# Kernel tuning notes

Hardware: AMD Instinct MI355X
Metric: run time of the kernel (lower is better)

The kernel has to match this reference:

```python
import jax, jax.numpy as jnp
import numpy as np

D_MODEL = 1024
NHEAD = 16
D_FF = 4096
LN_EPS = 1e-5


def _layer_norm(x, g, b):
    mu = jnp.mean(x, axis=-1, keepdims=True)
    var = jnp.mean(jnp.square(x - mu), axis=-1, keepdims=True)
    return (x - mu) * jax.lax.rsqrt(var + LN_EPS) * g + b


def setup_inputs() -> dict:
    key = jax.random.key(0)
    ks = jax.random.split(key, 12)
    d, f = D_MODEL, D_FF
    s = 1.0 / np.sqrt(d)
    inp = {
        "src": jax.random.normal(ks[0], (2, 2048, d), dtype=jnp.float32),
        "Wq": jax.random.uniform(ks[1], (d, d), jnp.float32, -s, s),
        "bq": jnp.zeros((d,), jnp.float32),
        "Wk": jax.random.uniform(ks[2], (d, d), jnp.float32, -s, s),
        "bk": jnp.zeros((d,), jnp.float32),
        "Wv": jax.random.uniform(ks[3], (d, d), jnp.float32, -s, s),
        "bv": jnp.zeros((d,), jnp.float32),
        "Wo": jax.random.uniform(ks[4], (d, d), jnp.float32, -s, s),
        "bo": jnp.zeros((d,), jnp.float32),
        "W1": jax.random.uniform(ks[5], (d, f), jnp.float32, -s, s),
        "b1": jnp.zeros((f,), jnp.float32),
        "W2": jax.random.uniform(ks[6], (f, d), jnp.float32, -1.0 / np.sqrt(f), 1.0 / np.sqrt(f)),
        "b2": jnp.zeros((d,), jnp.float32),
        "ln1_g": jnp.ones((d,), jnp.float32),
        "ln1_b": jnp.zeros((d,), jnp.float32),
        "ln2_g": jnp.ones((d,), jnp.float32),
        "ln2_b": jnp.zeros((d,), jnp.float32),
    }
    return inp


def reference(src, Wq, bq, Wk, bk, Wv, bv, Wo, bo, W1, b1, W2, b2,
              ln1_g, ln1_b, ln2_g, ln2_b):
    B, S, D = src.shape
    H = NHEAD
    hd = D // H
    # QKV projections, split into heads: [B, H, S, hd]
    q = (src @ Wq + bq).reshape(B, S, H, hd).transpose(0, 2, 1, 3)
    k = (src @ Wk + bk).reshape(B, S, H, hd).transpose(0, 2, 1, 3)
    v = (src @ Wv + bv).reshape(B, S, H, hd).transpose(0, 2, 1, 3)
    # Explicit full-score attention (no mask branch), as in source.
    scores = jnp.einsum("bhqd,bhkd->bhqk", q, k) / jnp.sqrt(jnp.asarray(hd, src.dtype))
    attn = jax.nn.softmax(scores, axis=-1)
    ctx = jnp.einsum("bhqk,bhkd->bhqd", attn, v)
    ctx = ctx.transpose(0, 2, 1, 3).reshape(B, S, D)
    src2 = ctx @ Wo + bo
    x = _layer_norm(src + src2, ln1_g, ln1_b)
    ff = jax.nn.relu(x @ W1 + b1) @ W2 + b2
    out = _layer_norm(x + ff, ln2_g, ln2_b)
    return out
```

## Files before the change

### kernel.cpp

```cpp
#include <hip/hip_runtime.h>
#include <cstdint>
#include <cstddef>

#define SEQ 2048
#define BATCH 2
#define ROWS (BATCH * SEQ)

typedef __attribute__((ext_vector_type(8))) short short8;
typedef __attribute__((ext_vector_type(4))) float f32x4;
typedef __attribute__((ext_vector_type(8))) _Float16 half8;
typedef __attribute__((ext_vector_type(2))) __fp16 fp16x2;

__device__ __forceinline__ unsigned short f2bf(float f) {
  union { float f; uint32_t u; } v; v.f = f;
  uint32_t r = v.u + 0x7fffu + ((v.u >> 16) & 1u);
  return (unsigned short)(r >> 16);
}

__device__ __forceinline__ unsigned short bf2h(unsigned short b) {
  union { uint32_t u; float f; } v; v.u = ((uint32_t)b) << 16;
  union { _Float16 h; unsigned short u; } o; o.h = (_Float16)v.f;
  return o.u;
}

__device__ __forceinline__ void async16(const void* g, void* l) {
  __builtin_amdgcn_global_load_lds((const __attribute__((address_space(1))) void*)g,
                                   (__attribute__((address_space(3))) void*)l, 16, 0, 0);
}

__global__ __launch_bounds__(256) void f2bf_kernel(const float* __restrict__ in,
                                                   unsigned short* __restrict__ out) {
  size_t i = ((size_t)blockIdx.x * 256 + threadIdx.x) * 4;
  float4 vv = *(const float4*)(in + i);
  ushort4 o;
  o.x = f2bf(vv.x); o.y = f2bf(vv.y); o.z = f2bf(vv.z); o.w = f2bf(vv.w);
  *(ushort4*)(out + i) = o;
}

__global__ __launch_bounds__(256) void wtrans(const float* __restrict__ W,
                                              unsigned short* __restrict__ WT,
                                              int K, int N, float scale) {
  __shared__ float t[32][33];
  int n0 = blockIdx.x * 32, k0 = blockIdx.y * 32;
  for (int i = threadIdx.y; i < 32; i += 8)
    t[i][threadIdx.x] = W[(size_t)(k0 + i) * N + n0 + threadIdx.x];
  __syncthreads();
  for (int i = threadIdx.y; i < 32; i += 8)
    WT[(size_t)(n0 + i) * K + k0 + threadIdx.x] = f2bf(t[threadIdx.x][i] * scale);
}

__global__ __launch_bounds__(256) void bias_concat(const float* __restrict__ bq,
                                                   const float* __restrict__ bk,
                                                   const float* __restrict__ bv,
                                                   float* __restrict__ o) {
  int i = blockIdx.x * 256 + threadIdx.x;
  float v = (i < 1024) ? bq[i] * 0.18033688f : (i < 2048 ? bk[i - 1024] : bv[i - 2048]);
  o[i] = v;
}

__global__ __launch_bounds__(256) void vtrans(const unsigned short* __restrict__ qkv,
                                              unsigned short* __restrict__ VT) {
  const int st = blockIdx.x, bh = blockIdx.y, b = bh >> 4, h = bh & 15;
  __shared__ unsigned short t[64][72];
  const int tid = threadIdx.x;
#pragma unroll
  for (int it = 0; it < 2; ++it) {
    int i = it * 256 + tid;
    int s = i >> 3, c = (i & 7) * 8;
    short8 v = *(const short8*)(qkv + ((size_t)b * SEQ + st * 64 + s) * 3072 + 2048 + h * 64 + c);
#pragma unroll
    for (int j = 0; j < 8; ++j) t[c + j][s] = bf2h((unsigned short)v[j]);
  }
  __syncthreads();
#pragma unroll
  for (int it = 0; it < 2; ++it) {
    int i = it * 256 + tid;
    int d = i >> 3, sc = (i & 7) * 8;
    short8 o;
#pragma unroll
    for (int j = 0; j < 8; ++j) o[j] = (short)t[d][sc + j];
    *(short8*)(VT + ((size_t)bh * 64 + d) * 2048 + st * 64 + sc) = o;
  }
}

template <bool RELU, bool OUTBF, bool HASRES>
__global__ __launch_bounds__(256) void gemm_bt(
    const unsigned short* __restrict__ A, const unsigned short* __restrict__ BT,
    const float* __restrict__ bias, const float* __restrict__ Rres,
    float* __restrict__ outF, unsigned short* __restrict__ outB,
    int M, int N, int K) {
  __shared__ unsigned short As[2][128 * 32];
  __shared__ unsigned short Bs[2][128 * 32];
  const int tid = threadIdx.x;
  const int lane = tid & 63, ln = lane & 15, quad = lane >> 4;
  const int w = tid >> 6;
  const int m0 = blockIdx.y * 128, n0 = blockIdx.x * 128;
  const int mw = (w >> 1) * 64, nw = (w & 1) * 64;
  f32x4 acc[4][4] = {};
  const int i0 = tid, i1 = tid + 256;
  const int r0 = i0 >> 2, kc0 = (i0 & 3) * 8;
  const int r1 = i1 >> 2, kc1 = (i1 & 3) * 8;
  for (int k0 = 0; k0 < K; k0 += 64) {
    __syncthreads();
#pragma unroll
    for (int p = 0; p < 2; ++p) {
      const int kp = k0 + p * 32;
      async16(A + (size_t)(m0 + r0) * K + kp + kc0, &As[p][i0 * 8]);
      async16(A + (size_t)(m0 + r1) * K + kp + kc1, &As[p][i1 * 8]);
      async16(BT + (size_t)(n0 + r0) * K + kp + kc0, &Bs[p][i0 * 8]);
      async16(BT + (size_t)(n0 + r1) * K + kp + kc1, &Bs[p][i1 * 8]);
    }
    __syncthreads();
#pragma unroll
    for (int p = 0; p < 2; ++p) {
      short8 a[4], b[4];
#pragma unroll
      for (int mi = 0; mi < 4; ++mi)
        a[mi] = *(const short8*)&As[p][(mw + mi * 16 + ln) * 32 + quad * 8];
#pragma unroll
      for (int ni = 0; ni < 4; ++ni)
        b[ni] = *(const short8*)&Bs[p][(nw + ni * 16 + ln) * 32 + quad * 8];
#pragma unroll
      for (int mi = 0; mi < 4; ++mi)
#pragma unroll
        for (int ni = 0; ni < 4; ++ni)
          acc[mi][ni] = __builtin_amdgcn_mfma_f32_16x16x32_bf16(a[mi], b[ni], acc[mi][ni], 0, 0, 0);
    }
  }
#pragma unroll
  for (int mi = 0; mi < 4; ++mi) {
#pragma unroll
    for (int ni = 0; ni < 4; ++ni) {
#pragma unroll
      for (int reg = 0; reg < 4; ++reg) {
        int row = m0 + mw + mi * 16 + quad * 4 + reg;
        int col = n0 + nw + ni * 16 + ln;
        float v = acc[mi][ni][reg] + bias[col];
        if (HASRES) v += Rres[(size_t)row * N + col];
        if (RELU) v = fmaxf(v, 0.f);
        if (OUTBF) outB[(size_t)row * N + col] = f2bf(v);
        else outF[(size_t)row * N + col] = v;
      }
    }
  }
}

template <bool RELU, bool OUTBF, bool HASRES>
__global__ __launch_bounds__(256) void gemm_bt64(
    const unsigned short* __restrict__ A, const unsigned short* __restrict__ BT,
    const float* __restrict__ bias, const float* __restrict__ Rres,
    float* __restrict__ outF, unsigned short* __restrict__ outB,
    int M, int N, int K) {
  __shared__ unsigned short As[4][128 * 32];
  __shared__ unsigned short Bs[4][64 * 32];
  const int tid = threadIdx.x;
  const int lane = tid & 63, ln = lane & 15, quad = lane >> 4;
  const int w = tid >> 6;
  const int m0 = blockIdx.y * 128, n0 = blockIdx.x * 64;
  const int mw = w * 32;
  f32x4 acc[2][4] = {};
  const int i0 = tid, i1 = tid + 256;
  const int r0 = i0 >> 2, kc0 = (i0 & 3) * 8;
  const int r1 = i1 >> 2, kc1 = (i1 & 3) * 8;
  for (int k0 = 0; k0 < K; k0 += 128) {
    __syncthreads();
#pragma unroll
    for (int p = 0; p < 4; ++p) {
      const int kp = k0 + p * 32;
      async16(A + (size_t)(m0 + r0) * K + kp + kc0, &As[p][i0 * 8]);
      async16(A + (size_t)(m0 + r1) * K + kp + kc1, &As[p][i1 * 8]);
      async16(BT + (size_t)(n0 + r0) * K + kp + kc0, &Bs[p][i0 * 8]);
    }
    __syncthreads();
#pragma unroll
    for (int p = 0; p < 4; ++p) {
      short8 a[2], b[4];
#pragma unroll
      for (int mi = 0; mi < 2; ++mi)
        a[mi] = *(const short8*)&As[p][(mw + mi * 16 + ln) * 32 + quad * 8];
#pragma unroll
      for (int ni = 0; ni < 4; ++ni)
        b[ni] = *(const short8*)&Bs[p][(ni * 16 + ln) * 32 + quad * 8];
#pragma unroll
      for (int mi = 0; mi < 2; ++mi)
#pragma unroll
        for (int ni = 0; ni < 4; ++ni)
          acc[mi][ni] = __builtin_amdgcn_mfma_f32_16x16x32_bf16(a[mi], b[ni], acc[mi][ni], 0, 0, 0);
    }
  }
#pragma unroll
  for (int mi = 0; mi < 2; ++mi) {
#pragma unroll
    for (int ni = 0; ni < 4; ++ni) {
#pragma unroll
      for (int reg = 0; reg < 4; ++reg) {
        int row = m0 + mw + mi * 16 + quad * 4 + reg;
        int col = n0 + ni * 16 + ln;
        float v = acc[mi][ni][reg] + bias[col];
        if (HASRES) v += Rres[(size_t)row * N + col];
        if (RELU) v = fmaxf(v, 0.f);
        if (OUTBF) outB[(size_t)row * N + col] = f2bf(v);
        else outF[(size_t)row * N + col] = v;
      }
    }
  }
}

__global__ __launch_bounds__(256, 4) void attn_kernel(const unsigned short* __restrict__ qkv,
                                                      const unsigned short* __restrict__ VT,
                                                      unsigned short* __restrict__ ctx) {
  const int qt = blockIdx.x;
  const int bh = blockIdx.y, b = bh >> 4, h = bh & 15;
  const int tid = threadIdx.x;
  const int w = tid >> 6, lane = tid & 63, ln = lane & 15, quad = lane >> 4;
  __shared__ __align__(16) unsigned short Ks[2 * 4096];
  __shared__ __align__(16) unsigned short Vs[2 * 4096];
  __shared__ __align__(16) unsigned short Ps[4096];
  const size_t rowbase = (size_t)b * SEQ;
  const unsigned short* kbase = qkv + (rowbase)*3072 + 1024 + h * 64;
  const unsigned short* vbase = VT + (size_t)bh * 64 * 2048;
  const int r0 = tid >> 3, c0 = tid & 7;
  const int r1 = r0 + 32;
  const int sw0 = r0 * 64 + ((c0 ^ (r0 & 7)) * 8);
  const int sw1 = r1 * 64 + ((c0 ^ (r1 & 7)) * 8);
  const int lh = ln & 7;
  const int qrow = w * 16 + ln;
  const unsigned short* qb = qkv + (rowbase + qt * 64) * 3072 + h * 64;
  short8 aq0 = *(const short8*)(qb + (size_t)qrow * 3072 + quad * 8);
  short8 aq1 = *(const short8*)(qb + (size_t)qrow * 3072 + 32 + quad * 8);
  short8 kreg0 = *(const short8*)(kbase + (size_t)r0 * 3072 + c0 * 8);
  short8 kreg1 = *(const short8*)(kbase + (size_t)r1 * 3072 + c0 * 8);
  short8 vreg0 = *(const short8*)(vbase + (size_t)r0 * 2048 + c0 * 8);
  short8 vreg1 = *(const short8*)(vbase + (size_t)r1 * 2048 + c0 * 8);
  *(short8*)&Ks[sw0] = kreg0;
  *(short8*)&Ks[sw1] = kreg1;
  *(short8*)&Vs[sw0] = vreg0;
  *(short8*)&Vs[sw1] = vreg1;
  __syncthreads();
  f32x4 oacc[4] = {};
  float lsum[4] = {};
  const int pr0 = ln * 64 + ((0 + quad) ^ lh) * 8;
  const int pr1 = ln * 64 + ((4 + quad) ^ lh) * 8;
  unsigned short* Pw = &Ps[w * 1024];
  int bsel = 0;
  for (int kt = 0; kt < 32; ++kt) {
    if (kt < 31) {
      const unsigned short* kp = kbase + (size_t)(kt + 1) * 64 * 3072;
      const unsigned short* vp = vbase + (kt + 1) * 64;
      kreg0 = *(const short8*)(kp + (size_t)r0 * 3072 + c0 * 8);
      kreg1 = *(const short8*)(kp + (size_t)r1 * 3072 + c0 * 8);
      vreg0 = *(const short8*)(vp + (size_t)r0 * 2048 + c0 * 8);
      vreg1 = *(const short8*)(vp + (size_t)r1 * 2048 + c0 * 8);
    }
    const unsigned short* Kb = &Ks[bsel];
    const unsigned short* Vb = &Vs[bsel];
#pragma unroll
    for (int nt = 0; nt < 4; ++nt) {
      short8 bk0 = *(const short8*)&Kb[(nt * 16 + ln) * 64 + ((0 + quad) ^ lh) * 8];
      short8 bk1 = *(const short8*)&Kb[(nt * 16 + ln) * 64 + ((4 + quad) ^ lh) * 8];
      const int pc = nt * 2 + (ln >> 3);
      const int q4 = quad * 4;
      f32x4 z = {};
      __builtin_amdgcn_s_setprio(1);
      z = __builtin_amdgcn_mfma_f32_16x16x32_bf16(aq0, bk0, z, 0, 0, 0);
      z = __builtin_amdgcn_mfma_f32_16x16x32_bf16(aq1, bk1, z, 0, 0, 0);
      __builtin_amdgcn_s_setprio(0);
      float p0 = __builtin_amdgcn_exp2f(z[0]);
      float p1 = __builtin_amdgcn_exp2f(z[1]);
      float p2 = __builtin_amdgcn_exp2f(z[2]);
      float p3 = __builtin_amdgcn_exp2f(z[3]);
      lsum[0] += p0; lsum[1] += p1; lsum[2] += p2; lsum[3] += p3;
      union { fp16x2 h; unsigned short u[2]; } ca, cb;
      ca.h = __builtin_amdgcn_cvt_pkrtz(p0, p1);
      cb.h = __builtin_amdgcn_cvt_pkrtz(p2, p3);
      Pw[(q4 + 0) * 64 + ((pc ^ ((q4 + 0) & 7)) * 8) + lh] = ca.u[0];
      Pw[(q4 + 1) * 64 + ((pc ^ ((q4 + 1) & 7)) * 8) + lh] = ca.u[1];
      Pw[(q4 + 2) * 64 + ((pc ^ ((q4 + 2) & 7)) * 8) + lh] = cb.u[0];
      Pw[(q4 + 3) * 64 + ((pc ^ ((q4 + 3) & 7)) * 8) + lh] = cb.u[1];
    }
    asm volatile("s_waitcnt lgkmcnt(0)" ::: "memory");
    half8 ap0 = *(const half8*)&Pw[pr0];
    half8 ap1 = *(const half8*)&Pw[pr1];
#pragma unroll
    for (int ot = 0; ot < 4; ++ot) {
      half8 bv0 = *(const half8*)&Vb[(ot * 16 + ln) * 64 + ((0 + quad) ^ lh) * 8];
      half8 bv1 = *(const half8*)&Vb[(ot * 16 + ln) * 64 + ((4 + quad) ^ lh) * 8];
      __builtin_amdgcn_s_setprio(1);
      oacc[ot] = __builtin_amdgcn_mfma_f32_16x16x32_f16(ap0, bv0, oacc[ot], 0, 0, 0);
      oacc[ot] = __builtin_amdgcn_mfma_f32_16x16x32_f16(ap1, bv1, oacc[ot], 0, 0, 0);
      __builtin_amdgcn_s_setprio(0);
    }
    if (kt < 31) {
      bsel ^= 4096;
      *(short8*)&Ks[bsel + sw0] = kreg0;
      *(short8*)&Ks[bsel + sw1] = kreg1;
      *(short8*)&Vs[bsel + sw0] = vreg0;
      *(short8*)&Vs[bsel + sw1] = vreg1;
      __syncthreads();
    }
  }
  {
    float rl[4];
#pragma unroll
    for (int r = 0; r < 4; ++r) {
      float l = lsum[r];
#pragma unroll
      for (int off = 1; off < 16; off <<= 1) l += __shfl_xor(l, off);
      rl[r] = 1.0f / l;
    }
#pragma unroll
    for (int ot = 0; ot < 4; ++ot)
#pragma unroll
      for (int r = 0; r < 4; ++r) {
        int srow = qt * 64 + w * 16 + quad * 4 + r;
        int c = h * 64 + ot * 16 + ln;
        ctx[(rowbase + srow) * 1024 + c] = f2bf(oacc[ot][r] * rl[r]);
      }
  }
}

__global__ __launch_bounds__(256) void ln_kernel(const float* __restrict__ y,
                                                 const float* __restrict__ g,
                                                 const float* __restrict__ bb,
                                                 float* __restrict__ outF,
                                                 unsigned short* __restrict__ outB) {
  const int row = blockIdx.x;
  const int tid = threadIdx.x;
  const float* yr = y + (size_t)row * 1024;
  float v[4]; float s = 0.f, s2 = 0.f;
#pragma unroll
  for (int j = 0; j < 4; ++j) {
    v[j] = yr[tid + j * 256];
    s += v[j]; s2 += v[j] * v[j];
  }
#pragma unroll
  for (int off = 1; off < 64; off <<= 1) {
    s += __shfl_xor(s, off);
    s2 += __shfl_xor(s2, off);
  }
  __shared__ float ws1[4], ws2[4];
  if ((tid & 63) == 0) { ws1[tid >> 6] = s; ws2[tid >> 6] = s2; }
  __syncthreads();
  s = ws1[0] + ws1[1] + ws1[2] + ws1[3];
  s2 = ws2[0] + ws2[1] + ws2[2] + ws2[3];
  const float mu = s * (1.f / 1024.f);
  const float var = s2 * (1.f / 1024.f) - mu * mu;
  const float rstd = rsqrtf(var + 1e-5f);
#pragma unroll
  for (int j = 0; j < 4; ++j) {
    int c = tid + j * 256;
    float val = (v[j] - mu) * rstd * g[c] + bb[c];
    if (outF) outF[(size_t)row * 1024 + c] = val;
    if (outB) outB[(size_t)row * 1024 + c] = f2bf(val);
  }
}

extern "C" void kernel_launch(void* const* d_in, const int* in_sizes, int n_in,
                              void* d_out, int out_size, void* d_ws, size_t ws_size,
                              hipStream_t stream) {
  const float* src = (const float*)d_in[0];
  const float* Wq = (const float*)d_in[1];
  const float* bq = (const float*)d_in[2];
  const float* Wk = (const float*)d_in[3];
  const float* bk = (const float*)d_in[4];
  const float* Wv = (const float*)d_in[5];
  const float* bv = (const float*)d_in[6];
  const float* Wo = (const float*)d_in[7];
  const float* bo = (const float*)d_in[8];
  const float* W1 = (const float*)d_in[9];
  const float* b1 = (const float*)d_in[10];
  const float* W2 = (const float*)d_in[11];
  const float* b2 = (const float*)d_in[12];
  const float* ln1g = (const float*)d_in[13];
  const float* ln1b = (const float*)d_in[14];
  const float* ln2g = (const float*)d_in[15];
  const float* ln2b = (const float*)d_in[16];
  float* out = (float*)d_out;

  char* ws = (char*)d_ws;
  unsigned short* qkvT = (unsigned short*)(ws + 0);
  unsigned short* WoT  = (unsigned short*)(ws + 6291456);
  unsigned short* W1T  = (unsigned short*)(ws + 8388608);
  unsigned short* W2T  = (unsigned short*)(ws + 16777216);
  float*          biasq = (float*)(ws + 25165824);
  unsigned short* xbf  = (unsigned short*)(ws + 25178112);
  unsigned short* qkv  = (unsigned short*)(ws + 33566720);
  unsigned short* hbuf = qkv;
  unsigned short* ctx  = (unsigned short*)(ws + 58732544);
  float*          ybuf = (float*)(ws + 67121152);
  unsigned short* VT   = (unsigned short*)(ws + 67121152);
  float*          xf   = (float*)(ws + 83898368);

  const float QSCALE = 0.18033688f;

  f2bf_kernel<<<4096, 256, 0, stream>>>(src, xbf);
  wtrans<<<dim3(32, 32), dim3(32, 8), 0, stream>>>(Wq, qkvT, 1024, 1024, QSCALE);
  wtrans<<<dim3(32, 32), dim3(32, 8), 0, stream>>>(Wk, qkvT + 1024 * 1024, 1024, 1024, 1.0f);
  wtrans<<<dim3(32, 32), dim3(32, 8), 0, stream>>>(Wv, qkvT + 2048 * 1024, 1024, 1024, 1.0f);
  wtrans<<<dim3(32, 32), dim3(32, 8), 0, stream>>>(Wo, WoT, 1024, 1024, 1.0f);
  wtrans<<<dim3(128, 32), dim3(32, 8), 0, stream>>>(W1, W1T, 1024, 4096, 1.0f);
  wtrans<<<dim3(32, 128), dim3(32, 8), 0, stream>>>(W2, W2T, 4096, 1024, 1.0f);
  bias_concat<<<12, 256, 0, stream>>>(bq, bk, bv, biasq);

  gemm_bt<false, true, false><<<dim3(24, 32), 256, 0, stream>>>(
      xbf, qkvT, biasq, nullptr, nullptr, qkv, ROWS, 3072, 1024);
  vtrans<<<dim3(32, 32), 256, 0, stream>>>(qkv, VT);
  attn_kernel<<<dim3(32, 32), 256, 0, stream>>>(qkv, VT, ctx);
  gemm_bt64<false, false, true><<<dim3(16, 32), 256, 0, stream>>>(
      ctx, WoT, bo, src, ybuf, nullptr, ROWS, 1024, 1024);
  ln_kernel<<<4096, 256, 0, stream>>>(ybuf, ln1g, ln1b, xf, xbf);
  gemm_bt<true, true, false><<<dim3(32, 32), 256, 0, stream>>>(
      xbf, W1T, b1, nullptr, nullptr, hbuf, ROWS, 4096, 1024);
  gemm_bt64<false, false, true><<<dim3(16, 32), 256, 0, stream>>>(
      hbuf, W2T, b2, xf, ybuf, nullptr, ROWS, 1024, 4096);
  ln_kernel<<<4096, 256, 0, stream>>>(ybuf, ln2g, ln2b, out, nullptr);
}
```

Baseline: 394.1 us.

## Rewrite attention with 32x32 MFMA, transposed scores and register-resident P

The attention kernel switches from 16x16x32 MFMAs with 4 waves per 64-query tile to 32x32x16 MFMAs with 2 waves, each owning 32 query rows. It computes S^T = K·Q^T so each lane holds the scores for its own query column. The exponentiated probabilities then go straight into the PV MFMA operand via v_permlane32_swap, which removes the LDS round trip for P. This cuts LDS traffic and synchronisation, at the cost of fewer waves per block, more registers per thread and heavier K/V staging per thread.

```diff
diff --git a/kernel.cpp b/kernel.cpp
--- a/kernel.cpp
+++ b/kernel.cpp
@@ -8,6 +8,7 @@
 
 typedef __attribute__((ext_vector_type(8))) short short8;
 typedef __attribute__((ext_vector_type(4))) float f32x4;
+typedef __attribute__((ext_vector_type(16))) float f32x16;
 typedef __attribute__((ext_vector_type(8))) _Float16 half8;
 typedef __attribute__((ext_vector_type(2))) __fp16 fp16x2;
 
@@ -206,116 +207,124 @@
   }
 }
 
-__global__ __launch_bounds__(256, 4) void attn_kernel(const unsigned short* __restrict__ qkv,
+__global__ __launch_bounds__(128, 2) void attn_kernel(const unsigned short* __restrict__ qkv,
                                                       const unsigned short* __restrict__ VT,
                                                       unsigned short* __restrict__ ctx) {
   const int qt = blockIdx.x;
   const int bh = blockIdx.y, b = bh >> 4, h = bh & 15;
   const int tid = threadIdx.x;
-  const int w = tid >> 6, lane = tid & 63, ln = lane & 15, quad = lane >> 4;
+  const int w = tid >> 6, lane = tid & 63;
+  const int r32 = lane & 31, hi = lane >> 5, r7 = r32 & 7;
   __shared__ __align__(16) unsigned short Ks[2 * 4096];
   __shared__ __align__(16) unsigned short Vs[2 * 4096];
-  __shared__ __align__(16) unsigned short Ps[4096];
   const size_t rowbase = (size_t)b * SEQ;
-  const unsigned short* kbase = qkv + (rowbase)*3072 + 1024 + h * 64;
+  const unsigned short* kbase = qkv + rowbase * 3072 + 1024 + h * 64;
   const unsigned short* vbase = VT + (size_t)bh * 64 * 2048;
-  const int r0 = tid >> 3, c0 = tid & 7;
-  const int r1 = r0 + 32;
-  const int sw0 = r0 * 64 + ((c0 ^ (r0 & 7)) * 8);
-  const int sw1 = r1 * 64 + ((c0 ^ (r1 & 7)) * 8);
-  const int lh = ln & 7;
-  const int qrow = w * 16 + ln;
-  const unsigned short* qb = qkv + (rowbase + qt * 64) * 3072 + h * 64;
-  short8 aq0 = *(const short8*)(qb + (size_t)qrow * 3072 + quad * 8);
-  short8 aq1 = *(const short8*)(qb + (size_t)qrow * 3072 + 32 + quad * 8);
-  short8 kreg0 = *(const short8*)(kbase + (size_t)r0 * 3072 + c0 * 8);
-  short8 kreg1 = *(const short8*)(kbase + (size_t)r1 * 3072 + c0 * 8);
-  short8 vreg0 = *(const short8*)(vbase + (size_t)r0 * 2048 + c0 * 8);
-  short8 vreg1 = *(const short8*)(vbase + (size_t)r1 * 2048 + c0 * 8);
-  *(short8*)&Ks[sw0] = kreg0;
-  *(short8*)&Ks[sw1] = kreg1;
-  *(short8*)&Vs[sw0] = vreg0;
-  *(short8*)&Vs[sw1] = vreg1;
+  int r_[4], s_[4], wsw_[4];
+#pragma unroll
+  for (int i = 0; i < 4; ++i) {
+    int idx = i * 128 + tid;
+    r_[i] = idx >> 3; s_[i] = idx & 7;
+    wsw_[i] = r_[i] * 64 + ((s_[i] ^ (r_[i] & 7)) * 8);
+  }
+  short8 qf[4];
+  {
+    const unsigned short* qp = qkv + (rowbase + qt * 64 + w * 32 + r32) * 3072 + h * 64;
+#pragma unroll
+    for (int dc = 0; dc < 4; ++dc) qf[dc] = *(const short8*)(qp + dc * 16 + hi * 8);
+  }
+  short8 kst[4], vst[4];
+#pragma unroll
+  for (int i = 0; i < 4; ++i) {
+    kst[i] = *(const short8*)(kbase + (size_t)r_[i] * 3072 + s_[i] * 8);
+    vst[i] = *(const short8*)(vbase + (size_t)r_[i] * 2048 + s_[i] * 8);
+  }
+#pragma unroll
+  for (int i = 0; i < 4; ++i) {
+    *(short8*)&Ks[wsw_[i]] = kst[i];
+    *(short8*)&Vs[wsw_[i]] = vst[i];
+  }
   __syncthreads();
-  f32x4 oacc[4] = {};
-  float lsum[4] = {};
-  const int pr0 = ln * 64 + ((0 + quad) ^ lh) * 8;
-  const int pr1 = ln * 64 + ((4 + quad) ^ lh) * 8;
-  unsigned short* Pw = &Ps[w * 1024];
-  int bsel = 0;
+  f32x16 oacc0 = {}, oacc1 = {};
+  float lsum = 0.f;
+  int cur = 0;
   for (int kt = 0; kt < 32; ++kt) {
     if (kt < 31) {
       const unsigned short* kp = kbase + (size_t)(kt + 1) * 64 * 3072;
       const unsigned short* vp = vbase + (kt + 1) * 64;
-      kreg0 = *(const short8*)(kp + (size_t)r0 * 3072 + c0 * 8);
-      kreg1 = *(const short8*)(kp + (size_t)r1 * 3072 + c0 * 8);
-      vreg0 = *(const short8*)(vp + (size_t)r0 * 2048 + c0 * 8);
-      vreg1 = *(const short8*)(vp + (size_t)r1 * 2048 + c0 * 8);
-    }
-    const unsigned short* Kb = &Ks[bsel];
-    const unsigned short* Vb = &Vs[bsel];
-#pragma unroll
-    for (int nt = 0; nt < 4; ++nt) {
-      short8 bk0 = *(const short8*)&Kb[(nt * 16 + ln) * 64 + ((0 + quad) ^ lh) * 8];
-      short8 bk1 = *(const short8*)&Kb[(nt * 16 + ln) * 64 + ((4 + quad) ^ lh) * 8];
-      const int pc = nt * 2 + (ln >> 3);
-      const int q4 = quad * 4;
-      f32x4 z = {};
-      __builtin_amdgcn_s_setprio(1);
-      z = __builtin_amdgcn_mfma_f32_16x16x32_bf16(aq0, bk0, z, 0, 0, 0);
-      z = __builtin_amdgcn_mfma_f32_16x16x32_bf16(aq1, bk1, z, 0, 0, 0);
-      __builtin_amdgcn_s_setprio(0);
-      float p0 = __builtin_amdgcn_exp2f(z[0]);
-      float p1 = __builtin_amdgcn_exp2f(z[1]);
-      float p2 = __builtin_amdgcn_exp2f(z[2]);
-      float p3 = __builtin_amdgcn_exp2f(z[3]);
-      lsum[0] += p0; lsum[1] += p1; lsum[2] += p2; lsum[3] += p3;
-      union { fp16x2 h; unsigned short u[2]; } ca, cb;
-      ca.h = __builtin_amdgcn_cvt_pkrtz(p0, p1);
-      cb.h = __builtin_amdgcn_cvt_pkrtz(p2, p3);
-      Pw[(q4 + 0) * 64 + ((pc ^ ((q4 + 0) & 7)) * 8) + lh] = ca.u[0];
-      Pw[(q4 + 1) * 64 + ((pc ^ ((q4 + 1) & 7)) * 8) + lh] = ca.u[1];
-      Pw[(q4 + 2) * 64 + ((pc ^ ((q4 + 2) & 7)) * 8) + lh] = cb.u[0];
-      Pw[(q4 + 3) * 64 + ((pc ^ ((q4 + 3) & 7)) * 8) + lh] = cb.u[1];
-    }
-    asm volatile("s_waitcnt lgkmcnt(0)" ::: "memory");
-    half8 ap0 = *(const half8*)&Pw[pr0];
-    half8 ap1 = *(const half8*)&Pw[pr1];
-#pragma unroll
-    for (int ot = 0; ot < 4; ++ot) {
-      half8 bv0 = *(const half8*)&Vb[(ot * 16 + ln) * 64 + ((0 + quad) ^ lh) * 8];
-      half8 bv1 = *(const half8*)&Vb[(ot * 16 + ln) * 64 + ((4 + quad) ^ lh) * 8];
-      __builtin_amdgcn_s_setprio(1);
-      oacc[ot] = __builtin_amdgcn_mfma_f32_16x16x32_f16(ap0, bv0, oacc[ot], 0, 0, 0);
-      oacc[ot] = __builtin_amdgcn_mfma_f32_16x16x32_f16(ap1, bv1, oacc[ot], 0, 0, 0);
-      __builtin_amdgcn_s_setprio(0);
-    }
+#pragma unroll
+      for (int i = 0; i < 4; ++i) {
+        kst[i] = *(const short8*)(kp + (size_t)r_[i] * 3072 + s_[i] * 8);
+        vst[i] = *(const short8*)(vp + (size_t)r_[i] * 2048 + s_[i] * 8);
+      }
+    }
+    const unsigned short* Kb = &Ks[cur];
+    const unsigned short* Vb = &Vs[cur];
+    f32x16 z0 = {}, z1 = {};
+    __builtin_amdgcn_s_setprio(1);
+#pragma unroll
+    for (int dc = 0; dc < 4; ++dc) {
+      const int sl = ((dc * 2 + hi) ^ r7) * 8;
+      short8 kf0 = *(const short8*)&Kb[r32 * 64 + sl];
+      short8 kf1 = *(const short8*)&Kb[(32 + r32) * 64 + sl];
+      z0 = __builtin_amdgcn_mfma_f32_32x32x16_bf16(kf0, qf[dc], z0, 0, 0, 0);
+      z1 = __builtin_amdgcn_mfma_f32_32x32x16_bf16(kf1, qf[dc], z1, 0, 0, 0);
+    }
+    __builtin_amdgcn_s_setprio(0);
+    half8 pf[4];
+#pragma unroll
+    for (int kc = 0; kc < 4; ++kc) {
+      float e[8];
+#pragma unroll
+      for (int j = 0; j < 8; ++j) {
+        float zz = (kc < 2) ? z0[(kc & 1) * 8 + j] : z1[(kc & 1) * 8 + j];
+        e[j] = __builtin_amdgcn_exp2f(zz);
+        lsum += e[j];
+      }
+      union { fp16x2 hh; unsigned int u; } a0, a1, b0, b1;
+      a0.hh = __builtin_amdgcn_cvt_pkrtz(e[0], e[1]);
+      a1.hh = __builtin_amdgcn_cvt_pkrtz(e[2], e[3]);
+      b0.hh = __builtin_amdgcn_cvt_pkrtz(e[4], e[5]);
+      b1.hh = __builtin_amdgcn_cvt_pkrtz(e[6], e[7]);
+      asm volatile("v_permlane32_swap_b32 %0, %1" : "+v"(a0.u), "+v"(b0.u));
+      asm volatile("v_permlane32_swap_b32 %0, %1" : "+v"(a1.u), "+v"(b1.u));
+      union { unsigned int u[4]; half8 hh; } fr;
+      fr.u[0] = a0.u; fr.u[1] = a1.u; fr.u[2] = b0.u; fr.u[3] = b1.u;
+      pf[kc] = fr.hh;
+    }
+    __builtin_amdgcn_s_setprio(1);
+#pragma unroll
+    for (int kc = 0; kc < 4; ++kc) {
+      const int sl = ((kc * 2 + hi) ^ r7) * 8;
+      half8 vf0 = *(const half8*)&Vb[r32 * 64 + sl];
+      half8 vf1 = *(const half8*)&Vb[(32 + r32) * 64 + sl];
+      oacc0 = __builtin_amdgcn_mfma_f32_32x32x16_f16(vf0, pf[kc], oacc0, 0, 0, 0);
+      oacc1 = __builtin_amdgcn_mfma_f32_32x32x16_f16(vf1, pf[kc], oacc1, 0, 0, 0);
+    }
+    __builtin_amdgcn_s_setprio(0);
     if (kt < 31) {
-      bsel ^= 4096;
-      *(short8*)&Ks[bsel + sw0] = kreg0;
-      *(short8*)&Ks[bsel + sw1] = kreg1;
-      *(short8*)&Vs[bsel + sw0] = vreg0;
-      *(short8*)&Vs[bsel + sw1] = vreg1;
+      const int nb = cur ^ 4096;
+#pragma unroll
+      for (int i = 0; i < 4; ++i) {
+        *(short8*)&Ks[nb + wsw_[i]] = kst[i];
+        *(short8*)&Vs[nb + wsw_[i]] = vst[i];
+      }
       __syncthreads();
-    }
-  }
-  {
-    float rl[4];
-#pragma unroll
-    for (int r = 0; r < 4; ++r) {
-      float l = lsum[r];
-#pragma unroll
-      for (int off = 1; off < 16; off <<= 1) l += __shfl_xor(l, off);
-      rl[r] = 1.0f / l;
-    }
-#pragma unroll
-    for (int ot = 0; ot < 4; ++ot)
-#pragma unroll
-      for (int r = 0; r < 4; ++r) {
-        int srow = qt * 64 + w * 16 + quad * 4 + r;
-        int c = h * 64 + ot * 16 + ln;
-        ctx[(rowbase + srow) * 1024 + c] = f2bf(oacc[ot][r] * rl[r]);
-      }
+      cur = nb;
+    }
+  }
+  float tot = lsum + __shfl_xor(lsum, 32);
+  float rl = 1.0f / tot;
+  const size_t orow = (rowbase + (size_t)qt * 64 + w * 32 + r32) * 1024 + h * 64 + hi * 4;
+#pragma unroll
+  for (int tq = 0; tq < 4; ++tq) {
+    ushort4 o0, o1;
+    o0.x = f2bf(oacc0[tq * 4 + 0] * rl); o0.y = f2bf(oacc0[tq * 4 + 1] * rl);
+    o0.z = f2bf(oacc0[tq * 4 + 2] * rl); o0.w = f2bf(oacc0[tq * 4 + 3] * rl);
+    *(ushort4*)(ctx + orow + tq * 8) = o0;
+    o1.x = f2bf(oacc1[tq * 4 + 0] * rl); o1.y = f2bf(oacc1[tq * 4 + 1] * rl);
+    o1.z = f2bf(oacc1[tq * 4 + 2] * rl); o1.w = f2bf(oacc1[tq * 4 + 3] * rl);
+    *(ushort4*)(ctx + orow + 32 + tq * 8) = o1;
   }
 }
 
@@ -405,7 +414,7 @@
   gemm_bt<false, true, false><<<dim3(24, 32), 256, 0, stream>>>(
       xbf, qkvT, biasq, nullptr, nullptr, qkv, ROWS, 3072, 1024);
   vtrans<<<dim3(32, 32), 256, 0, stream>>>(qkv, VT);
-  attn_kernel<<<dim3(32, 32), 256, 0, stream>>>(qkv, VT, ctx);
+  attn_kernel<<<dim3(32, 32), 128, 0, stream>>>(qkv, VT, ctx);
   gemm_bt64<false, false, true><<<dim3(16, 32), 256, 0, stream>>>(
       ctx, WoT, bo, src, ybuf, nullptr, ROWS, 1024, 1024);
   ln_kernel<<<4096, 256, 0, stream>>>(ybuf, ln1g, ln1b, xf, xbf);
```

After: 393.5 us. About the same (-0.2%).
